# Performance work log

Measured on AMD Instinct MI355X. Metric: run time of the kernel, lower is better.

## Reference

```python
import jax, jax.numpy as jnp
import numpy as np

WIN = 11          # win_size
NC = 2            # num_classes
SMOOTH = 0.1      # smoothing / (num_classes - 1) = 0.1/1; fix_flag=True and 0.1 <= Max_Smootning=0.2


def setup_inputs() -> dict:
    key = jax.random.key(0)
    k1, k2 = jax.random.split(key)
    x = jax.random.normal(k1, (8, 2, 1024, 1024), dtype=jnp.float32)
    target = jax.random.randint(k2, (8, 1, 1024, 1024), 0, 2, dtype=jnp.int32)
    return {"x": x, "target": target}


def reference(x, target):
    kern = -jnp.ones((1, 1, WIN, WIN), dtype=jnp.float32)
    kern = kern.at[0, 0, WIN // 2, WIN // 2].set(float(WIN * WIN - 1))

    tf = target.astype(jnp.float32)  # [B,1,H,W]
    pad = WIN // 2
    edge = jax.lax.conv_general_dilated(tf, kern, window_strides=(1, 1),
                                        padding=[(pad, pad), (pad, pad)])
    edge = jnp.where(edge != 0, 1.0, 0.0)  # [B,1,H,W], 1 near label edges

    log_p = jax.nn.log_softmax(x, axis=1)  # [B,C,H,W]

    # One-hot masks (to_categorical with alpha=0 and alpha=smoothing).
    oh = jax.nn.one_hot(target[:, 0], NC, dtype=jnp.float32)  # [B,H,W,C]
    oh = jnp.transpose(oh, (0, 3, 1, 2))                      # [B,C,H,W]
    # alpha everywhere, 1 - alpha + alpha/NC at the true class
    soft = SMOOTH + oh * (1.0 - 2.0 * SMOOTH + SMOOTH / NC)

    mask = oh * (1.0 - edge) + soft * edge  # hard label off-edge, smoothed on-edge
    loss = jnp.mean(jnp.sum(mask * log_p, axis=1))
    return -loss
```

## Files before the change

### kernel.cpp

```cpp
#include <hip/hip_runtime.h>

#define HH 1024
#define WW 1024
#define BB 8
#define WORDS_X 16
#define NPART 4096

__global__ __launch_bounds__(256) void ls_edge(const int* __restrict__ tgt,
                                               unsigned long long* __restrict__ eb,
                                               unsigned long long* __restrict__ tb) {
    __shared__ unsigned long long s_w[74][3];
    __shared__ unsigned long long s_oh[74], s_ah[74];

    const int tid  = threadIdx.x;
    const int lane = tid & 63;
    const int wv   = tid >> 6;
    const int b  = blockIdx.z;
    const int ty = blockIdx.y * 64;
    const int tx = blockIdx.x * 64;
    const int* tp = tgt + (size_t)b * HH * WW;

    for (int task = wv; task < 74 * 3; task += 4) {
        int r = task / 3, k = task - 3 * r;
        int gy = ty - 5 + r;
        int gx = tx + (k - 1) * 64 + lane;
        int v = 0;
        if ((unsigned)gy < HH && (unsigned)gx < WW) v = tp[(size_t)gy * WW + gx];
        unsigned long long m = __ballot(v != 0);
        if (lane == 0) s_w[r][k] = m;
    }
    __syncthreads();

    if (tid < 74) {
        unsigned long long wl = s_w[tid][0], wm = s_w[tid][1], wr = s_w[tid][2];
        unsigned long long oh = wm, ah = wm;
#pragma unroll
        for (int d = 1; d <= 5; ++d) {
            unsigned long long vr = (wm >> d) | (wr << (64 - d));
            unsigned long long vl = (wm << d) | (wl >> (64 - d));
            oh |= vr | vl;
            ah &= vr & vl;
        }
        s_oh[tid] = oh;
        s_ah[tid] = ah;
    }
    __syncthreads();

    if (tid < 64) {
        unsigned long long ov = 0, av = ~0ULL;
#pragma unroll
        for (int k = 0; k < 11; ++k) { ov |= s_oh[tid + k]; av &= s_ah[tid + k]; }
        unsigned long long tc = s_w[tid + 5][1];
        unsigned long long e  = (ov & ~tc) | (~av & tc);
        size_t w = (size_t)((b << 10) + ty + tid) * WORDS_X + blockIdx.x;
        eb[w] = e;
        tb[w] = tc;
    }
}

__global__ __launch_bounds__(256) void ls_loss(const float* __restrict__ x,
                                               const unsigned long long* __restrict__ eb,
                                               const unsigned long long* __restrict__ tb,
                                               float* __restrict__ partial) {
    __shared__ float s_red[4];
    const int tid = threadIdx.x;
    const int blk = blockIdx.x;
    const int b   = blk >> 9;
    const int off = ((blk & 511) << 11) + (tid << 3);

    const float* x0p = x + (size_t)b * 2 * HH * WW + off;
    const float* x1p = x0p + (size_t)HH * WW;
    float4 a0 = ((const float4*)x0p)[0], a1 = ((const float4*)x0p)[1];
    float4 b0 = ((const float4*)x1p)[0], b1 = ((const float4*)x1p)[1];

    size_t widx = ((size_t)b * HH * WW + off) >> 6;
    unsigned int sh = off & 63;
    unsigned int e8 = (unsigned int)(eb[widx] >> sh) & 0xffu;
    unsigned int t8 = (unsigned int)(tb[widx] >> sh) & 0xffu;

    float f0[8] = {a0.x, a0.y, a0.z, a0.w, a1.x, a1.y, a1.z, a1.w};
    float f1[8] = {b0.x, b0.y, b0.z, b0.w, b1.x, b1.y, b1.z, b1.w};

    float acc = 0.f;
#pragma unroll
    for (int j = 0; j < 8; ++j) {
        int t = (t8 >> j) & 1;
        int e = (e8 >> j) & 1;
        float v0 = f0[j], v1 = f1[j];
        float m   = fmaxf(v0, v1);
        float lse = m + __logf(1.0f + __expf(-fabsf(v0 - v1)));
        float lp0 = v0 - lse, lp1 = v1 - lse;
        float lpt = t ? lp1 : lp0;
        float lpo = t ? lp0 : lp1;
        acc += e ? (0.95f * lpt + 0.1f * lpo) : lpt;
    }

#pragma unroll
    for (int offl = 32; offl > 0; offl >>= 1) acc += __shfl_down(acc, offl, 64);
    if ((tid & 63) == 0) s_red[tid >> 6] = acc;
    __syncthreads();
    if (tid == 0) partial[blk] = s_red[0] + s_red[1] + s_red[2] + s_red[3];
}

__global__ __launch_bounds__(256) void ls_final(const float* __restrict__ partial,
                                                float* __restrict__ out) {
    __shared__ double s_red[4];
    const int tid = threadIdx.x;
    double s = 0.0;
    for (int i = tid; i < NPART; i += 256) s += (double)partial[i];
#pragma unroll
    for (int off = 32; off > 0; off >>= 1) s += __shfl_down(s, off, 64);
    if ((tid & 63) == 0) s_red[tid >> 6] = s;
    __syncthreads();
    if (tid == 0) {
        double total = s_red[0] + s_red[1] + s_red[2] + s_red[3];
        out[0] = (float)(-total * (1.0 / (8.0 * 1024.0 * 1024.0)));
    }
}

extern "C" void kernel_launch(void* const* d_in, const int* in_sizes, int n_in,
                              void* d_out, int out_size, void* d_ws, size_t ws_size,
                              hipStream_t stream) {
    const float* x  = (const float*)d_in[0];
    const int* tgt  = (const int*)d_in[1];

    float* partial = (float*)d_ws;
    unsigned long long* eb = (unsigned long long*)((char*)d_ws + (64 << 10));
    unsigned long long* tb = eb + (size_t)BB * HH * WORDS_X;

    hipLaunchKernelGGL(ls_edge, dim3(16, 16, 8), dim3(256), 0, stream, tgt, eb, tb);
    hipLaunchKernelGGL(ls_loss, dim3(NPART), dim3(256), 0, stream, x, eb, tb, partial);
    hipLaunchKernelGGL(ls_final, dim3(1), dim3(256), 0, stream, partial, (float*)d_out);
}
```

Before: 143.3 us.

## Pack target bits separately and fuse edge computation into tiled loss kernel

```diff
diff --git a/kernel.cpp b/kernel.cpp
--- a/kernel.cpp
+++ b/kernel.cpp
@@ -4,40 +4,77 @@
 #define WW 1024
 #define BB 8
 #define WORDS_X 16
-#define NPART 4096
+#define NPART 2048
 
-__global__ __launch_bounds__(256) void ls_edge(const int* __restrict__ tgt,
-                                               unsigned long long* __restrict__ eb,
-                                               unsigned long long* __restrict__ tb) {
-    __shared__ unsigned long long s_w[74][3];
-    __shared__ unsigned long long s_oh[74], s_ah[74];
+typedef unsigned long long u64;
 
-    const int tid  = threadIdx.x;
-    const int lane = tid & 63;
-    const int wv   = tid >> 6;
+__global__ __launch_bounds__(256) void ls_pack(const int* __restrict__ tgt,
+                                               u64* __restrict__ bits) {
+    const int lane = threadIdx.x & 63;
+    const size_t wv = ((size_t)blockIdx.x * 256 + threadIdx.x) >> 6;
+    const size_t wbase = wv * 8;
+    const int* p = tgt + wbase * 64 + lane;
+
+    int v[8];
+#pragma unroll
+    for (int j = 0; j < 8; ++j) v[j] = p[j * 64];
+
+    u64 mine = 0;
+#pragma unroll
+    for (int j = 0; j < 8; ++j) {
+        u64 m = __ballot(v[j] != 0);
+        if (lane == j) mine = m;
+    }
+    if (lane < 8) bits[wbase + lane] = mine;
+}
+
+__global__ __launch_bounds__(256) void ls_loss(const float* __restrict__ x,
+                                               const u64* __restrict__ bits,
+                                               float* __restrict__ partial) {
+    __shared__ u64 s_w[74][3];
+    __shared__ u64 s_oh[74], s_ah[74], s_e[64];
+    __shared__ float s_red[4];
+
+    const int tid = threadIdx.x;
     const int b  = blockIdx.z;
     const int ty = blockIdx.y * 64;
-    const int tx = blockIdx.x * 64;
-    const int* tp = tgt + (size_t)b * HH * WW;
+    const int wx = blockIdx.x;
 
-    for (int task = wv; task < 74 * 3; task += 4) {
-        int r = task / 3, k = task - 3 * r;
+    const int row = tid >> 2;
+    const int c0  = (tid & 3) << 4;
+    const float* x0p = x + ((size_t)b * 2 + 0) * HH * WW
+                         + (size_t)(ty + row) * WW + (wx << 6) + c0;
+    const float* x1p = x0p + (size_t)HH * WW;
+    float4 xv0[4], xv1[4];
+#pragma unroll
+    for (int q = 0; q < 4; ++q) xv0[q] = ((const float4*)x0p)[q];
+#pragma unroll
+    for (int q = 0; q < 4; ++q) xv1[q] = ((const float4*)x1p)[q];
+
+    if (tid < 222) {
+        int r = tid / 3, k = tid - 3 * r;
         int gy = ty - 5 + r;
-        int gx = tx + (k - 1) * 64 + lane;
-        int v = 0;
-        if ((unsigned)gy < HH && (unsigned)gx < WW) v = tp[(size_t)gy * WW + gx];
-        unsigned long long m = __ballot(v != 0);
-        if (lane == 0) s_w[r][k] = m;
+        int wi = wx - 1 + k;
+        u64 v = 0;
+        if ((unsigned)gy < HH && (unsigned)wi < WORDS_X)
+            v = bits[((size_t)(b << 10) + gy) * WORDS_X + wi];
+        s_w[r][k] = v;
+    }
+
+#pragma unroll
+    for (int q = 0; q < 4; ++q) {
+        asm volatile("" :: "v"(xv0[q].x), "v"(xv0[q].y), "v"(xv0[q].z), "v"(xv0[q].w));
+        asm volatile("" :: "v"(xv1[q].x), "v"(xv1[q].y), "v"(xv1[q].z), "v"(xv1[q].w));
     }
     __syncthreads();
 
     if (tid < 74) {
-        unsigned long long wl = s_w[tid][0], wm = s_w[tid][1], wr = s_w[tid][2];
-        unsigned long long oh = wm, ah = wm;
+        u64 wl = s_w[tid][0], wm = s_w[tid][1], wr = s_w[tid][2];
+        u64 oh = wm, ah = wm;
 #pragma unroll
         for (int d = 1; d <= 5; ++d) {
-            unsigned long long vr = (wm >> d) | (wr << (64 - d));
-            unsigned long long vl = (wm << d) | (wl >> (64 - d));
+            u64 vr = (wm >> d) | (wr << (64 - d));
+            u64 vl = (wm << d) | (wl >> (64 - d));
             oh |= vr | vl;
             ah &= vr & vl;
         }
@@ -47,45 +84,24 @@
     __syncthreads();
 
     if (tid < 64) {
-        unsigned long long ov = 0, av = ~0ULL;
+        u64 ov = 0, av = ~0ULL;
 #pragma unroll
         for (int k = 0; k < 11; ++k) { ov |= s_oh[tid + k]; av &= s_ah[tid + k]; }
-        unsigned long long tc = s_w[tid + 5][1];
-        unsigned long long e  = (ov & ~tc) | (~av & tc);
-        size_t w = (size_t)((b << 10) + ty + tid) * WORDS_X + blockIdx.x;
-        eb[w] = e;
-        tb[w] = tc;
+        u64 tc = s_w[tid + 5][1];
+        s_e[tid] = (ov & ~tc) | (~av & tc);
     }
-}
+    __syncthreads();
 
-__global__ __launch_bounds__(256) void ls_loss(const float* __restrict__ x,
-                                               const unsigned long long* __restrict__ eb,
-                                               const unsigned long long* __restrict__ tb,
-                                               float* __restrict__ partial) {
-    __shared__ float s_red[4];
-    const int tid = threadIdx.x;
-    const int blk = blockIdx.x;
-    const int b   = blk >> 9;
-    const int off = ((blk & 511) << 11) + (tid << 3);
+    unsigned int e16 = (unsigned int)(s_e[row] >> c0) & 0xffffu;
+    unsigned int t16 = (unsigned int)(s_w[row + 5][1] >> c0) & 0xffffu;
 
-    const float* x0p = x + (size_t)b * 2 * HH * WW + off;
-    const float* x1p = x0p + (size_t)HH * WW;
-    float4 a0 = ((const float4*)x0p)[0], a1 = ((const float4*)x0p)[1];
-    float4 b0 = ((const float4*)x1p)[0], b1 = ((const float4*)x1p)[1];
-
-    size_t widx = ((size_t)b * HH * WW + off) >> 6;
-    unsigned int sh = off & 63;
-    unsigned int e8 = (unsigned int)(eb[widx] >> sh) & 0xffu;
-    unsigned int t8 = (unsigned int)(tb[widx] >> sh) & 0xffu;
-
-    float f0[8] = {a0.x, a0.y, a0.z, a0.w, a1.x, a1.y, a1.z, a1.w};
-    float f1[8] = {b0.x, b0.y, b0.z, b0.w, b1.x, b1.y, b1.z, b1.w};
-
+    const float* f0 = (const float*)xv0;
+    const float* f1 = (const float*)xv1;
     float acc = 0.f;
 #pragma unroll
-    for (int j = 0; j < 8; ++j) {
-        int t = (t8 >> j) & 1;
-        int e = (e8 >> j) & 1;
+    for (int j = 0; j < 16; ++j) {
+        int t = (t16 >> j) & 1;
+        int e = (e16 >> j) & 1;
         float v0 = f0[j], v1 = f1[j];
         float m   = fmaxf(v0, v1);
         float lse = m + __logf(1.0f + __expf(-fabsf(v0 - v1)));
@@ -96,10 +112,13 @@
     }
 
 #pragma unroll
-    for (int offl = 32; offl > 0; offl >>= 1) acc += __shfl_down(acc, offl, 64);
+    for (int off = 32; off > 0; off >>= 1) acc += __shfl_down(acc, off, 64);
     if ((tid & 63) == 0) s_red[tid >> 6] = acc;
     __syncthreads();
-    if (tid == 0) partial[blk] = s_red[0] + s_red[1] + s_red[2] + s_red[3];
+    if (tid == 0) {
+        int bid = (blockIdx.z * gridDim.y + blockIdx.y) * gridDim.x + blockIdx.x;
+        partial[bid] = s_red[0] + s_red[1] + s_red[2] + s_red[3];
+    }
 }
 
 __global__ __launch_bounds__(256) void ls_final(const float* __restrict__ partial,
@@ -125,10 +144,9 @@
     const int* tgt  = (const int*)d_in[1];
 
     float* partial = (float*)d_ws;
-    unsigned long long* eb = (unsigned long long*)((char*)d_ws + (64 << 10));
-    unsigned long long* tb = eb + (size_t)BB * HH * WORDS_X;
+    u64* bits = (u64*)((char*)d_ws + (16 << 10));
 
-    hipLaunchKernelGGL(ls_edge, dim3(16, 16, 8), dim3(256), 0, stream, tgt, eb, tb);
-    hipLaunchKernelGGL(ls_loss, dim3(NPART), dim3(256), 0, stream, x, eb, tb, partial);
+    hipLaunchKernelGGL(ls_pack, dim3(4096), dim3(256), 0, stream, tgt, bits);
+    hipLaunchKernelGGL(ls_loss, dim3(16, 16, 8), dim3(256), 0, stream, x, bits, partial);
     hipLaunchKernelGGL(ls_final, dim3(1), dim3(256), 0, stream, partial, (float*)d_out);
 }
```

New measurement: 118.6 us. 17.3% less time.
